# Kernel optimization log

Measured on AMD Instinct MI355X. Metric: run time of the kernel, lower is better.

Reference implementation:

```python
import jax, jax.numpy as jnp
import numpy as np

N_EDGES = 1048576
N_CENTERS = 32768
N_SPECIES = 4
L_MAX = 3
N_BASIS = 12
N_MAX = 8
R_CUT = 5.0
NORM = 1.0 / np.sqrt(32.0)  # hypers['normalize'] = avg_num_neighbors = 32
SH_SPLITS = [0, 1, 4, 9, 16]  # cumulative offsets of (2l+1)


def real_sph_harm_lmax3(u):
    # u: [E,3] unit vectors; returns [E,16] real normalized spherical harmonics (sphericart order m=-l..l)
    x, y, z = u[:, 0], u[:, 1], u[:, 2]
    c0 = 0.5 * np.sqrt(1.0 / np.pi)
    c1 = np.sqrt(3.0 / (4.0 * np.pi))
    x2, y2, z2 = x * x, y * y, z * z
    sh = [
        jnp.full_like(x, c0),
        c1 * y, c1 * z, c1 * x,
        0.5 * np.sqrt(15.0 / np.pi) * x * y,
        0.5 * np.sqrt(15.0 / np.pi) * y * z,
        0.25 * np.sqrt(5.0 / np.pi) * (3.0 * z2 - 1.0),
        0.5 * np.sqrt(15.0 / np.pi) * x * z,
        0.25 * np.sqrt(15.0 / np.pi) * (x2 - y2),
        0.25 * np.sqrt(35.0 / (2.0 * np.pi)) * y * (3.0 * x2 - y2),
        0.5 * np.sqrt(105.0 / np.pi) * x * y * z,
        0.25 * np.sqrt(21.0 / (2.0 * np.pi)) * y * (5.0 * z2 - 1.0),
        0.25 * np.sqrt(7.0 / np.pi) * (5.0 * z2 * z - 3.0 * z),
        0.25 * np.sqrt(21.0 / (2.0 * np.pi)) * x * (5.0 * z2 - 1.0),
        0.25 * np.sqrt(105.0 / np.pi) * z * (x2 - y2),
        0.25 * np.sqrt(35.0 / (2.0 * np.pi)) * x * (x2 - y2),
    ]
    return jnp.stack(sh, axis=1)


def setup_inputs() -> dict:
    key = jax.random.key(0)
    k1, k2, k3, k4 = jax.random.split(key, 4)
    vectors = jax.random.normal(k1, (N_EDGES, 3), dtype=jnp.float32) * 1.5
    radial_weights = jax.random.normal(k2, (L_MAX + 1, N_BASIS, N_MAX), dtype=jnp.float32) * 0.1
    center_index = jax.random.randint(k3, (N_EDGES,), 0, N_CENTERS, dtype=jnp.int64)
    neighbor_species_index = jax.random.randint(k4, (N_EDGES,), 0, N_SPECIES, dtype=jnp.int64)
    return {"vectors": vectors, "radial_weights": radial_weights,
            "center_index": center_index, "neighbor_species_index": neighbor_species_index}


def reference(vectors, radial_weights, center_index, neighbor_species_index):
    # distances and unit vectors
    r = jnp.sqrt(jnp.sum(vectors * vectors, axis=-1) + 1e-12)  # [E]
    u = vectors / r[:, None]
    # smooth radial basis phi_n(r) = sin((n+1) pi r / r_cut)/r, normalized (LE-like)
    ns = jnp.arange(1, N_BASIS + 1, dtype=vectors.dtype)
    phi = jnp.sin(np.pi / R_CUT * r[:, None] * ns[None, :]) / r[:, None] * NORM  # [E, N_BASIS]
    sh = real_sph_harm_lmax3(u)  # [E,16]
    # scatter target: (center, neighbor_species) channel
    idx = center_index * N_SPECIES + neighbor_species_index  # [E]
    densities = []
    for l in range(L_MAX + 1):
        m_l = 2 * l + 1
        sh_l = jax.lax.slice_in_dim(sh, SH_SPLITS[l], SH_SPLITS[l + 1], axis=1)  # [E, 2l+1]
        rad_l = phi @ radial_weights[l]  # [E, N_MAX]
        edge_l = rad_l[:, None, :] * sh_l[:, :, None]  # [E, 2l+1, N_MAX] outer product
        dens = jax.ops.segment_sum(edge_l.reshape(edge_l.shape[0], -1), idx,
                                   num_segments=N_CENTERS * N_SPECIES)  # [N*S, m*n]
        dens = dens.reshape(N_CENTERS, N_SPECIES, m_l, N_MAX)
        dens = jnp.transpose(dens, (0, 2, 1, 3)).reshape(N_CENTERS, m_l, N_SPECIES * N_MAX)
        densities.append(dens)  # c^{a_i l}_{Ai, m, a_j n}
    # concatenate the per-l TensorMap blocks along the m axis -> [N, sum(2l+1), S*N_MAX]
    return jnp.concatenate(densities, axis=1)
```

## Files before the change

### kernel.cpp

```cpp
#include <hip/hip_runtime.h>
#include <math.h>

#define N_EDGES   1048576
#define N_BUCKET  1024
#define SEG_PER_B 128
#define N_BASIS   12
#define CAP       2048
#define HBLK      64
#define HEPB      (N_EDGES / HBLK)


#define WS_BLKHIST  0
#define WS_TOTALS   (HBLK * N_BUCKET * 4)
#define WS_OFFSETS  (WS_TOTALS + N_BUCKET * 4)
#define WS_RECORDS  (WS_OFFSETS + N_BUCKET * 4)
#define WS_NEEDED   (WS_RECORDS + N_EDGES * 4)

__device__ __forceinline__ void compute_edge(float x, float y, float z,
                                             float* __restrict__ ph,
                                             float* __restrict__ sh)
{
    const float r2    = fmaf(x, x, fmaf(y, y, z * z)) + 1e-12f;
    const float inv_r = rsqrtf(r2);
    const float r     = r2 * inv_r;
    x *= inv_r; y *= inv_r; z *= inv_r;

    const float t = 0.6283185307179586f * r;
    float s1, c1;
    __sincosf(t, &s1, &c1);
    const float twoc = 2.0f * c1;
    const float scale = 0.17677669529663687f * inv_r;
    float skm1 = 0.0f, sk = s1;
    #pragma unroll
    for (int b = 0; b < N_BASIS; ++b) {
        ph[b] = sk * scale;
        const float nxt = fmaf(twoc, sk, -skm1);
        skm1 = sk; sk = nxt;
    }

    const float x2 = x * x, y2 = y * y, z2 = z * z;
    sh[0]  = 0.28209479177387814f;
    sh[1]  = 0.4886025119029199f * y;
    sh[2]  = 0.4886025119029199f * z;
    sh[3]  = 0.4886025119029199f * x;
    sh[4]  = 1.0925484305920792f * x * y;
    sh[5]  = 1.0925484305920792f * y * z;
    sh[6]  = 0.31539156525252005f * (3.0f * z2 - 1.0f);
    sh[7]  = 1.0925484305920792f * x * z;
    sh[8]  = 0.5462742152960396f * (x2 - y2);
    sh[9]  = 0.5900435899266435f * y * (3.0f * x2 - y2);
    sh[10] = 2.890611442640554f  * x * y * z;
    sh[11] = 0.4570457994644658f * y * (5.0f * z2 - 1.0f);
    sh[12] = 0.3731763325901154f * (5.0f * z2 * z - 3.0f * z);
    sh[13] = 0.4570457994644658f * x * (5.0f * z2 - 1.0f);
    sh[14] = 1.445305721320277f  * z * (x2 - y2);
    sh[15] = 0.5900435899266435f * x * (x2 - y2);
}

__device__ __forceinline__ void accum_edge(const float4 v,
                                           const float (&Wn)[4][N_BASIS],
                                           float* __restrict__ acc)
{
    float ph[N_BASIS], sh[16];
    compute_edge(v.x, v.y, v.z, ph, sh);
    float rad[4];
    #pragma unroll
    for (int l = 0; l < 4; ++l) {
        float a = 0.0f;
        #pragma unroll
        for (int bb = 0; bb < N_BASIS; ++bb)
            a = fmaf(ph[bb], Wn[l][bb], a);
        rad[l] = a;
    }
    #pragma unroll
    for (int L = 0; L < 16; ++L) {
        const int l = (L == 0) ? 0 : (L < 4) ? 1 : (L < 9) ? 2 : 3;
        acc[L] = fmaf(sh[L], rad[l], acc[L]);
    }
}

__device__ __forceinline__ void flush_seg(const float* __restrict__ acc,
                                          int b, int sl, int n,
                                          float* __restrict__ out)
{
    const int seg = b * SEG_PER_B + sl;
    float* op = out + (size_t)(seg >> 2) * 512 + (seg & 3) * 8 + n;
    #pragma unroll
    for (int L = 0; L < 16; ++L) op[L * 32] = acc[L];
}

__global__ __launch_bounds__(1024) void hist_kernel(
    const int* __restrict__ cidx, const int* __restrict__ sidx,
    int* __restrict__ blkhist)
{
    __shared__ int h[N_BUCKET];
    const int t = threadIdx.x;
    h[t] = 0;
    __syncthreads();
    const int base = blockIdx.x * HEPB;
    #pragma unroll
    for (int k = 0; k < HEPB / 1024; ++k) {
        const int e = base + k * 1024 + t;
        const int seg = (cidx[e] << 2) | sidx[e];
        atomicAdd(&h[seg >> 7], 1);
    }
    __syncthreads();
    blkhist[blockIdx.x * N_BUCKET + t] = h[t];
}

__global__ __launch_bounds__(1024) void scan_kernel(
    int* __restrict__ blkhist, int* __restrict__ totals,
    int* __restrict__ offsets)
{
    __shared__ int tmp[N_BUCKET];
    const int t = threadIdx.x;
    int run = 0;
    for (int blk = 0; blk < HBLK; ++blk) {
        const int v = blkhist[blk * N_BUCKET + t];
        blkhist[blk * N_BUCKET + t] = run;
        run += v;
    }
    totals[t] = run;
    tmp[t] = run;
    __syncthreads();
    #pragma unroll
    for (int d = 1; d < N_BUCKET; d <<= 1) {
        const int v = (t >= d) ? tmp[t - d] : 0;
        __syncthreads();
        tmp[t] += v;
        __syncthreads();
    }
    offsets[t] = tmp[t] - run;
}

__global__ __launch_bounds__(1024) void partition_kernel(
    const int* __restrict__ cidx, const int* __restrict__ sidx,
    const int* __restrict__ blkhist, const int* __restrict__ offsets,
    unsigned int* __restrict__ records)
{
    __shared__ int bb[N_BUCKET];
    __shared__ int lcnt[N_BUCKET];
    const int t = threadIdx.x;
    bb[t]   = offsets[t] + blkhist[blockIdx.x * N_BUCKET + t];
    lcnt[t] = 0;
    __syncthreads();
    const int base = blockIdx.x * HEPB;
    #pragma unroll
    for (int k = 0; k < HEPB / 1024; ++k) {
        const int e = base + k * 1024 + t;
        const int seg = (cidx[e] << 2) | sidx[e];
        const int bkt = seg >> 7;
        const int r = atomicAdd(&lcnt[bkt], 1);
        records[bb[bkt] + r] = ((unsigned)(seg & 127) << 20) | (unsigned)e;
    }
}

__device__ __forceinline__ void compute_bucket(
    const unsigned int* __restrict__ sorted_rec, int off, int cnt, int b,
    const float* __restrict__ vectors, const float (&Wn)[4][N_BASIS],
    float* __restrict__ out,
    float4* __restrict__ pay, int* __restrict__ shist,
    int* __restrict__ soff, int* __restrict__ scur)
{
    const int t = threadIdx.x;
    const int n = t & 7;
    const int g = t >> 3;

    if (cnt > CAP) {
        #pragma unroll 1
        for (int k = 0; k < 4; ++k) {
            const int sl = g * 4 + k;
            float acc[16];
            #pragma unroll
            for (int L = 0; L < 16; ++L) acc[L] = 0.0f;
            for (int j = 0; j < cnt; ++j) {
                const unsigned rec = sorted_rec[off + j];
                if ((int)(rec >> 20) != sl) continue;
                const int eid = rec & 0xFFFFF;
                const float4 v = make_float4(vectors[3*eid], vectors[3*eid+1],
                                             vectors[3*eid+2], 0.0f);
                accum_edge(v, Wn, acc);
            }
            flush_seg(acc, b, sl, n, out);
        }
        return;
    }

    if (t < SEG_PER_B) shist[t] = 0;
    __syncthreads();

    unsigned recs[8];
    const int iters = (cnt + 255) >> 8;
    #pragma unroll
    for (int it = 0; it < 8; ++it) {
        const int i = it * 256 + t;
        if (it < iters && i < cnt) {
            recs[it] = sorted_rec[off + i];
            atomicAdd(&shist[recs[it] >> 20], 1);
        }
    }
    __syncthreads();

    if (t < SEG_PER_B) soff[t] = shist[t];
    __syncthreads();
    #pragma unroll
    for (int d = 1; d < SEG_PER_B; d <<= 1) {
        int v = 0;
        if (t >= d && t < SEG_PER_B) v = soff[t - d];
        __syncthreads();
        if (t < SEG_PER_B) soff[t] += v;
        __syncthreads();
    }
    if (t < SEG_PER_B) {
        const int ex = soff[t] - shist[t];
        soff[t] = ex;
        scur[t] = ex;
    }
    __syncthreads();

    #pragma unroll
    for (int it = 0; it < 8; ++it) {
        const int i = it * 256 + t;
        if (it < iters && i < cnt) {
            const unsigned rec = recs[it];
            const int sl  = rec >> 20;
            const int eid = rec & 0xFFFFF;
            const int r = atomicAdd(&scur[sl], 1);
            pay[r] = make_float4(vectors[3 * eid], vectors[3 * eid + 1],
                                 vectors[3 * eid + 2], __int_as_float(sl));
        }
    }
    __syncthreads();

    float* ob = out + (size_t)(b * 32 + g) * 512 + n;
    const int s0 = g * 4;
    #pragma unroll
    for (int kp = 0; kp < 2; ++kp) {
        float accA[16], accB[16];
        #pragma unroll
        for (int L = 0; L < 16; ++L) { accA[L] = 0.0f; accB[L] = 0.0f; }

        const int sA  = s0 + 2 * kp;
        const int jsA = soff[sA];
        const int jeA = soff[sA + 1];
        for (int j = jsA; j < jeA; ++j) accum_edge(pay[j], Wn, accA);

        const int sB  = sA + 1;
        const int jsB = soff[sB];
        const int jeB = (sB + 1 < SEG_PER_B) ? soff[sB + 1] : cnt;
        for (int j = jsB; j < jeB; ++j) accum_edge(pay[j], Wn, accB);

        #pragma unroll
        for (int L = 0; L < 16; ++L) {
            ob[L * 32 + (2 * kp) * 8]     = accA[L];
            ob[L * 32 + (2 * kp) * 8 + 8] = accB[L];
        }
    }
}

__global__ __launch_bounds__(256) void compute_kernel(
    const unsigned int* __restrict__ sorted_rec,
    const int* __restrict__ offsets, const int* __restrict__ counts,
    const float* __restrict__ vectors,
    const float* __restrict__ rw, float* __restrict__ out)
{
    __shared__ float4 pay[CAP];
    __shared__ int shist[SEG_PER_B];
    __shared__ int soff[SEG_PER_B];
    __shared__ int scur[SEG_PER_B];

    const int t = threadIdx.x;
    const int b = blockIdx.x;
    const int n = t & 7;

    float Wn[4][N_BASIS];
    #pragma unroll
    for (int l = 0; l < 4; ++l)
        #pragma unroll
        for (int bb = 0; bb < N_BASIS; ++bb)
            Wn[l][bb] = rw[(l * N_BASIS + bb) * 8 + n];

    compute_bucket(sorted_rec, offsets[b], counts[b], b, vectors, Wn, out,
                   pay, shist, soff, scur);
}

__global__ __launch_bounds__(256) void atomic_kernel(
    const float* __restrict__ vectors, const float* __restrict__ rw,
    const int* __restrict__ cidx, const int* __restrict__ sidx,
    float* __restrict__ out)
{
    const int e = blockIdx.x * 256 + threadIdx.x;
    if (e >= N_EDGES) return;
    float ph[N_BASIS], sh[16];
    compute_edge(vectors[3*e], vectors[3*e+1], vectors[3*e+2], ph, sh);
    float* op = out + (size_t)cidx[e] * 512 + sidx[e] * 8;
    for (int l = 0; l < 4; ++l) {
        const int L0 = l * l;
        const int ml = 2 * l + 1;
        for (int nn = 0; nn < 8; ++nn) {
            float rad = 0.0f;
            for (int bb = 0; bb < N_BASIS; ++bb)
                rad = fmaf(ph[bb], rw[(l * N_BASIS + bb) * 8 + nn], rad);
            for (int mm = 0; mm < ml; ++mm)
                atomicAdd(op + (L0 + mm) * 32 + nn, sh[L0 + mm] * rad);
        }
    }
}

extern "C" void kernel_launch(void* const* d_in, const int* in_sizes, int n_in,
                              void* d_out, int out_size, void* d_ws, size_t ws_size,
                              hipStream_t stream) {
    const float* vectors = (const float*)d_in[0];
    const float* rw      = (const float*)d_in[1];
    const int*   cidx    = (const int*)d_in[2];
    const int*   sidx    = (const int*)d_in[3];
    float*       out     = (float*)d_out;

    if (ws_size < (size_t)WS_NEEDED) {
        hipMemsetAsync(out, 0, (size_t)out_size * sizeof(float), stream);
        hipLaunchKernelGGL(atomic_kernel, dim3(N_EDGES / 256), dim3(256), 0, stream,
                           vectors, rw, cidx, sidx, out);
        return;
    }

    char* ws = (char*)d_ws;
    int*          blkhist = (int*)(ws + WS_BLKHIST);
    int*          totals  = (int*)(ws + WS_TOTALS);
    int*          offsets = (int*)(ws + WS_OFFSETS);
    unsigned int* records = (unsigned int*)(ws + WS_RECORDS);

    hipLaunchKernelGGL(hist_kernel,      dim3(HBLK),     dim3(1024), 0, stream, cidx, sidx, blkhist);
    hipLaunchKernelGGL(scan_kernel,      dim3(1),        dim3(1024), 0, stream, blkhist, totals, offsets);
    hipLaunchKernelGGL(partition_kernel, dim3(HBLK),     dim3(1024), 0, stream, cidx, sidx, blkhist, offsets, records);
    hipLaunchKernelGGL(compute_kernel,   dim3(N_BUCKET), dim3(256),  0, stream, records, offsets, totals, vectors, rw, out);
}
```

Measured before the change: 172.8 us.

## Fuse scan into partition kernel and use 512-thread compute blocks with two segments per group

Removes the single-block scan kernel: every partition block recomputes the per-bucket totals and its own prefix from the block histograms, and block 0 writes the global offsets and totals. The compute kernel becomes 512 threads per bucket, so each 8-thread group handles two segments instead of four. It walks the payload with a running segment id and flushes whenever the id changes, then writes zeros for empty segments. The shared payload capacity drops to 1280 entries to allow more blocks per CU, which sends more buckets to the slow overflow path. Each partition block also does redundant global reads of the histogram.

```diff
diff --git a/kernel.cpp b/kernel.cpp
--- a/kernel.cpp
+++ b/kernel.cpp
@@ -5,7 +5,7 @@
 #define N_BUCKET  1024
 #define SEG_PER_B 128
 #define N_BASIS   12
-#define CAP       2048
+#define CAP       1280
 #define HBLK      64
 #define HEPB      (N_EDGES / HBLK)
 
@@ -108,43 +108,40 @@
     blkhist[blockIdx.x * N_BUCKET + t] = h[t];
 }
 
-__global__ __launch_bounds__(1024) void scan_kernel(
-    int* __restrict__ blkhist, int* __restrict__ totals,
-    int* __restrict__ offsets)
-{
-    __shared__ int tmp[N_BUCKET];
-    const int t = threadIdx.x;
-    int run = 0;
+__global__ __launch_bounds__(1024) void partition_kernel(
+    const int* __restrict__ cidx, const int* __restrict__ sidx,
+    const int* __restrict__ blkhist,
+    unsigned int* __restrict__ records,
+    int* __restrict__ offsets_g, int* __restrict__ totals_g)
+{
+    __shared__ int scan_s[N_BUCKET];
+    __shared__ int bb[N_BUCKET];
+    __shared__ int lcnt[N_BUCKET];
+    const int t  = threadIdx.x;
+    const int me = blockIdx.x;
+
+    int total = 0, before = 0;
     for (int blk = 0; blk < HBLK; ++blk) {
         const int v = blkhist[blk * N_BUCKET + t];
-        blkhist[blk * N_BUCKET + t] = run;
-        run += v;
-    }
-    totals[t] = run;
-    tmp[t] = run;
+        total += v;
+        if (blk < me) before += v;
+    }
+    scan_s[t] = total;
     __syncthreads();
     #pragma unroll
     for (int d = 1; d < N_BUCKET; d <<= 1) {
-        const int v = (t >= d) ? tmp[t - d] : 0;
+        const int v = (t >= d) ? scan_s[t - d] : 0;
         __syncthreads();
-        tmp[t] += v;
+        scan_s[t] += v;
         __syncthreads();
     }
-    offsets[t] = tmp[t] - run;
-}
-
-__global__ __launch_bounds__(1024) void partition_kernel(
-    const int* __restrict__ cidx, const int* __restrict__ sidx,
-    const int* __restrict__ blkhist, const int* __restrict__ offsets,
-    unsigned int* __restrict__ records)
-{
-    __shared__ int bb[N_BUCKET];
-    __shared__ int lcnt[N_BUCKET];
-    const int t = threadIdx.x;
-    bb[t]   = offsets[t] + blkhist[blockIdx.x * N_BUCKET + t];
+    const int gbase = scan_s[t] - total;
+    bb[t]   = gbase + before;
     lcnt[t] = 0;
-    __syncthreads();
-    const int base = blockIdx.x * HEPB;
+    if (me == 0) { offsets_g[t] = gbase; totals_g[t] = total; }
+    __syncthreads();
+
+    const int base = me * HEPB;
     #pragma unroll
     for (int k = 0; k < HEPB / 1024; ++k) {
         const int e = base + k * 1024 + t;
@@ -155,21 +152,37 @@
     }
 }
 
-__device__ __forceinline__ void compute_bucket(
-    const unsigned int* __restrict__ sorted_rec, int off, int cnt, int b,
-    const float* __restrict__ vectors, const float (&Wn)[4][N_BASIS],
-    float* __restrict__ out,
-    float4* __restrict__ pay, int* __restrict__ shist,
-    int* __restrict__ soff, int* __restrict__ scur)
-{
+__global__ __launch_bounds__(512, 8) void compute_kernel(
+    const unsigned int* __restrict__ sorted_rec,
+    const int* __restrict__ offsets, const int* __restrict__ counts,
+    const float* __restrict__ vectors,
+    const float* __restrict__ rw,
+    float* __restrict__ out)
+{
+    __shared__ float4 pay[CAP];
+    __shared__ int shist[SEG_PER_B];
+    __shared__ int soff[SEG_PER_B + 1];
+    __shared__ int scur[SEG_PER_B];
+
     const int t = threadIdx.x;
+    const int b = blockIdx.x;
     const int n = t & 7;
     const int g = t >> 3;
 
+    float Wn[4][N_BASIS];
+    #pragma unroll
+    for (int l = 0; l < 4; ++l)
+        #pragma unroll
+        for (int bb = 0; bb < N_BASIS; ++bb)
+            Wn[l][bb] = rw[(l * N_BASIS + bb) * 8 + n];
+
+    const int off = offsets[b];
+    const int cnt = counts[b];
+
     if (cnt > CAP) {
         #pragma unroll 1
-        for (int k = 0; k < 4; ++k) {
-            const int sl = g * 4 + k;
+        for (int k = 0; k < 2; ++k) {
+            const int sl = g * 2 + k;
             float acc[16];
             #pragma unroll
             for (int L = 0; L < 16; ++L) acc[L] = 0.0f;
@@ -189,11 +202,11 @@
     if (t < SEG_PER_B) shist[t] = 0;
     __syncthreads();
 
-    unsigned recs[8];
-    const int iters = (cnt + 255) >> 8;
-    #pragma unroll
-    for (int it = 0; it < 8; ++it) {
-        const int i = it * 256 + t;
+    unsigned recs[3];
+    const int iters = (cnt + 511) >> 9;
+    #pragma unroll
+    for (int it = 0; it < 3; ++it) {
+        const int i = it * 512 + t;
         if (it < iters && i < cnt) {
             recs[it] = sorted_rec[off + i];
             atomicAdd(&shist[recs[it] >> 20], 1);
@@ -216,11 +229,12 @@
         soff[t] = ex;
         scur[t] = ex;
     }
-    __syncthreads();
-
-    #pragma unroll
-    for (int it = 0; it < 8; ++it) {
-        const int i = it * 256 + t;
+    if (t == SEG_PER_B) soff[SEG_PER_B] = cnt;
+    __syncthreads();
+
+    #pragma unroll
+    for (int it = 0; it < 3; ++it) {
+        const int i = it * 512 + t;
         if (it < iters && i < cnt) {
             const unsigned rec = recs[it];
             const int sl  = rec >> 20;
@@ -232,56 +246,40 @@
     }
     __syncthreads();
 
-    float* ob = out + (size_t)(b * 32 + g) * 512 + n;
-    const int s0 = g * 4;
-    #pragma unroll
-    for (int kp = 0; kp < 2; ++kp) {
-        float accA[16], accB[16];
-        #pragma unroll
-        for (int L = 0; L < 16; ++L) { accA[L] = 0.0f; accB[L] = 0.0f; }
-
-        const int sA  = s0 + 2 * kp;
-        const int jsA = soff[sA];
-        const int jeA = soff[sA + 1];
-        for (int j = jsA; j < jeA; ++j) accum_edge(pay[j], Wn, accA);
-
-        const int sB  = sA + 1;
-        const int jsB = soff[sB];
-        const int jeB = (sB + 1 < SEG_PER_B) ? soff[sB + 1] : cnt;
-        for (int j = jsB; j < jeB; ++j) accum_edge(pay[j], Wn, accB);
-
-        #pragma unroll
-        for (int L = 0; L < 16; ++L) {
-            ob[L * 32 + (2 * kp) * 8]     = accA[L];
-            ob[L * 32 + (2 * kp) * 8 + 8] = accB[L];
-        }
-    }
-}
-
-__global__ __launch_bounds__(256) void compute_kernel(
-    const unsigned int* __restrict__ sorted_rec,
-    const int* __restrict__ offsets, const int* __restrict__ counts,
-    const float* __restrict__ vectors,
-    const float* __restrict__ rw, float* __restrict__ out)
-{
-    __shared__ float4 pay[CAP];
-    __shared__ int shist[SEG_PER_B];
-    __shared__ int soff[SEG_PER_B];
-    __shared__ int scur[SEG_PER_B];
-
-    const int t = threadIdx.x;
-    const int b = blockIdx.x;
-    const int n = t & 7;
-
-    float Wn[4][N_BASIS];
-    #pragma unroll
-    for (int l = 0; l < 4; ++l)
-        #pragma unroll
-        for (int bb = 0; bb < N_BASIS; ++bb)
-            Wn[l][bb] = rw[(l * N_BASIS + bb) * 8 + n];
-
-    compute_bucket(sorted_rec, offsets[b], counts[b], b, vectors, Wn, out,
-                   pay, shist, soff, scur);
+    const int s0 = g * 2;
+    const int js = soff[s0];
+    const int je = soff[s0 + 2];
+
+    int cur = -1;
+    float acc[16];
+    #pragma unroll
+    for (int L = 0; L < 16; ++L) acc[L] = 0.0f;
+
+    for (int j = js; j < je; ++j) {
+        const float4 v = pay[j];
+        const int sl = __float_as_int(v.w);
+        if (sl != cur) {
+            if (cur >= 0) {
+                flush_seg(acc, b, cur, n, out);
+                #pragma unroll
+                for (int L = 0; L < 16; ++L) acc[L] = 0.0f;
+            }
+            cur = sl;
+        }
+        accum_edge(v, Wn, acc);
+    }
+    if (cur >= 0) flush_seg(acc, b, cur, n, out);
+
+    #pragma unroll
+    for (int k = 0; k < 2; ++k) {
+        const int sl = s0 + k;
+        if (shist[sl] == 0) {
+            float z[16];
+            #pragma unroll
+            for (int L = 0; L < 16; ++L) z[L] = 0.0f;
+            flush_seg(z, b, sl, n, out);
+        }
+    }
 }
 
 __global__ __launch_bounds__(256) void atomic_kernel(
@@ -330,7 +328,6 @@
     unsigned int* records = (unsigned int*)(ws + WS_RECORDS);
 
     hipLaunchKernelGGL(hist_kernel,      dim3(HBLK),     dim3(1024), 0, stream, cidx, sidx, blkhist);
-    hipLaunchKernelGGL(scan_kernel,      dim3(1),        dim3(1024), 0, stream, blkhist, totals, offsets);
-    hipLaunchKernelGGL(partition_kernel, dim3(HBLK),     dim3(1024), 0, stream, cidx, sidx, blkhist, offsets, records);
-    hipLaunchKernelGGL(compute_kernel,   dim3(N_BUCKET), dim3(256),  0, stream, records, offsets, totals, vectors, rw, out);
-}
+    hipLaunchKernelGGL(partition_kernel, dim3(HBLK),     dim3(1024), 0, stream, cidx, sidx, blkhist, records, offsets, totals);
+    hipLaunchKernelGGL(compute_kernel,   dim3(N_BUCKET), dim3(512),  0, stream, records, offsets, totals, vectors, rw, out);
+}
```

New measurement: 524.5 us. +203.6%, slower.
